# Performance work log

Hardware: AMD Instinct MI355X
Metric: run time of the kernel (lower is better)

## Reference

```python
import jax, jax.numpy as jnp
import numpy as np

B, N, D_IN, D_OUT, H = 64, 512, 256, 256, 4
HD = D_OUT // H


def setup_inputs() -> dict:
    key = jax.random.key(0)
    ks = jax.random.split(key, 10)
    x = jax.random.normal(ks[0], (B, N, D_IN), dtype=jnp.float32)
    adj = jax.random.randint(ks[1], (N, N), 0, 2, dtype=jnp.int32)
    adj = adj.at[jnp.arange(N), jnp.arange(N)].set(1)  # self-loops: no empty rows
    s_in = 1.0 / np.sqrt(D_IN)
    s_out = 1.0 / np.sqrt(D_OUT)
    wq = jax.random.uniform(ks[2], (D_OUT, D_IN), jnp.float32, -s_in, s_in)
    bq = jax.random.uniform(ks[3], (D_OUT,), jnp.float32, -s_in, s_in)
    wk = jax.random.uniform(ks[4], (D_OUT, D_IN), jnp.float32, -s_in, s_in)
    bk = jax.random.uniform(ks[5], (D_OUT,), jnp.float32, -s_in, s_in)
    wv = jax.random.uniform(ks[6], (D_OUT, D_IN), jnp.float32, -s_in, s_in)
    bv = jax.random.uniform(ks[7], (D_OUT,), jnp.float32, -s_in, s_in)
    wo = jax.random.uniform(ks[8], (D_OUT, D_OUT), jnp.float32, -s_out, s_out)
    bo = jax.random.uniform(ks[9], (D_OUT,), jnp.float32, -s_out, s_out)
    return {"x": x, "adj": adj, "wq": wq, "bq": bq, "wk": wk, "bk": bk,
            "wv": wv, "bv": bv, "wo": wo, "bo": bo}


def reference(x, adj, wq, bq, wk, bk, wv, bv, wo, bo):
    b, n, _ = x.shape
    # [B,N,D_out] -> [B,H,N,HD]
    q = (x @ wq.T + bq).reshape(b, n, H, HD).transpose(0, 2, 1, 3)
    k = (x @ wk.T + bk).reshape(b, n, H, HD).transpose(0, 2, 1, 3)
    v = (x @ wv.T + bv).reshape(b, n, H, HD).transpose(0, 2, 1, 3)
    scores = jnp.einsum('bhnd,bhmd->bhnm', q, k) / jnp.sqrt(jnp.float32(HD))
    scores = jnp.where(adj[None, None] == 0, -jnp.inf, scores)
    attn = jnp.nan_to_num(jax.nn.softmax(scores, axis=-1), nan=0.0)
    out = jnp.einsum('bhnm,bhmd->bhnd', attn, v)
    out = out.transpose(0, 2, 1, 3).reshape(b, n, D_OUT)
    return out @ wo.T + bo
```

## Files before the change

kernel.cpp:

```cpp
#include <hip/hip_runtime.h>
#include <stdint.h>

typedef float f32x4 __attribute__((ext_vector_type(4)));
typedef short s16x8 __attribute__((ext_vector_type(8)));
typedef unsigned short u16x4 __attribute__((ext_vector_type(4)));

#define BB 64
#define NN 512
#define DIN 256
#define DOUT 256
#define HH 4
#define HD 64

__device__ __forceinline__ unsigned short f2b(float f) {
  union { float f; unsigned u; } v; v.f = f;
  unsigned r = v.u + 0x7fffu + ((v.u >> 16) & 1u);
  return (unsigned short)(r >> 16);
}
__device__ __forceinline__ void mfma16(f32x4& acc, s16x8 a, s16x8 b) {
  acc = __builtin_amdgcn_mfma_f32_16x16x32_bf16(a, b, acc, 0, 0, 0);
}
__device__ __forceinline__ unsigned cvtpk(float lo, float hi) {
  unsigned r;
  asm("v_cvt_pk_bf16_f32 %0, %1, %2" : "=v"(r) : "v"(lo), "v"(hi));
  return r;
}

__global__ void k_conv(const float* __restrict__ src, unsigned short* __restrict__ dst, int n4) {
  int i = blockIdx.x * blockDim.x + threadIdx.x;
  if (i >= n4) return;
  f32x4 v = ((const f32x4*)src)[i];
  u16x4 o;
  o[0] = f2b(v[0]); o[1] = f2b(v[1]); o[2] = f2b(v[2]); o[3] = f2b(v[3]);
  ((u16x4*)dst)[i] = o;
}

__global__ void k_adjbits(const int* __restrict__ adj, unsigned long long* __restrict__ ab) {
  int row = blockIdx.x;
  int w = threadIdx.x >> 6, lane = threadIdx.x & 63;
  int v = adj[row * NN + w * 64 + lane];
  unsigned long long m = __ballot(v != 0);
  if (lane == 0) ab[row * 8 + w] = m;
}

__global__ __launch_bounds__(256) void k_qkv(
    const unsigned short* __restrict__ xh,
    const unsigned short* __restrict__ wqh,
    const unsigned short* __restrict__ wkh,
    const unsigned short* __restrict__ wvh,
    const float* __restrict__ bq, const float* __restrict__ bk, const float* __restrict__ bv,
    unsigned short* __restrict__ Qb, unsigned short* __restrict__ Kb, unsigned short* __restrict__ Vtb)
{
  __shared__ __align__(16) unsigned char xs[32768];
  __shared__ __align__(16) unsigned char wsl[32768];
  int tid = threadIdx.x, wave = tid >> 6, lane = tid & 63;
  int lr = lane & 15, lk = lane >> 4;
  int t0 = blockIdx.x * 64;
  int by = blockIdx.y, seg = by >> 2, nb0 = (by & 3) * 64;
  const unsigned short* wh = seg == 0 ? wqh : (seg == 1 ? wkh : wvh);
  const float* bias = seg == 0 ? bq : (seg == 1 ? bk : bv);
  int h = by & 3;

  const unsigned short* xsrc = xh + (size_t)t0 * DIN;
  const unsigned short* wsrc = wh + (size_t)nb0 * DIN;
#pragma unroll
  for (int i = 0; i < 8; ++i) {
    int lin = i * 256 + tid;
    int r = lin >> 5, c = lin & 31;
    int dst = r * 512 + ((c ^ (r & 7)) << 4);
    *(s16x8*)(xs + dst)  = *(const s16x8*)(xsrc + lin * 8);
    *(s16x8*)(wsl + dst) = *(const s16x8*)(wsrc + lin * 8);
  }
  __syncthreads();

  f32x4 acc[4] = {};
  if (seg < 2) {
    int chrow = wave * 16 + lr;
#pragma unroll
    for (int k0 = 0; k0 < 8; ++k0) {
      int cg = k0 * 4 + lk;
      s16x8 a = *(const s16x8*)(wsl + chrow * 512 + ((cg ^ (chrow & 7)) << 4));
#pragma unroll
      for (int ct = 0; ct < 4; ++ct) {
        int tr = ct * 16 + lr;
        s16x8 b = *(const s16x8*)(xs + tr * 512 + ((cg ^ (tr & 7)) << 4));
        mfma16(acc[ct], a, b);
      }
    }
    unsigned short* dst = (seg == 0) ? Qb : Kb;
    f32x4 bv4 = *(const f32x4*)(bias + nb0 + wave * 16 + lk * 4);
#pragma unroll
    for (int ct = 0; ct < 4; ++ct) {
      int n_ = t0 + ct * 16 + lr;
      int b_ = n_ >> 9, nn = n_ & 511;
      u16x4 pk;
#pragma unroll
      for (int j = 0; j < 4; ++j) pk[j] = f2b(acc[ct][j] + bv4[j]);
      *(u16x4*)(dst + ((size_t)(b_ * HH + h) * NN + nn) * HD + wave * 16 + lk * 4) = pk;
    }
  } else {
    int tokrow = wave * 16 + lr;
#pragma unroll
    for (int k0 = 0; k0 < 8; ++k0) {
      int cg = k0 * 4 + lk;
      s16x8 a = *(const s16x8*)(xs + tokrow * 512 + ((cg ^ (tokrow & 7)) << 4));
#pragma unroll
      for (int nt = 0; nt < 4; ++nt) {
        int cr = nt * 16 + lr;
        s16x8 b = *(const s16x8*)(wsl + cr * 512 + ((cg ^ (cr & 7)) << 4));
        mfma16(acc[nt], a, b);
      }
    }
    int m0 = t0 + wave * 16 + lk * 4;
    int b_ = m0 >> 9, n0 = m0 & 511;
#pragma unroll
    for (int nt = 0; nt < 4; ++nt) {
      int hd = nt * 16 + lr;
      float bs = bias[nb0 + hd];
      u16x4 pk;
#pragma unroll
      for (int j = 0; j < 4; ++j) pk[j] = f2b(acc[nt][j] + bs);
      *(u16x4*)(Vtb + ((size_t)(b_ * HH + h) * HD + hd) * NN + n0) = pk;
    }
  }
}

__global__ __launch_bounds__(256) void k_attn(
    const unsigned short* __restrict__ Qb, const unsigned short* __restrict__ Kb,
    const unsigned short* __restrict__ Vtb, const unsigned long long* __restrict__ ab,
    unsigned short* __restrict__ att)
{
  __shared__ __align__(16) unsigned char kl[8192];
  __shared__ __align__(16) unsigned char vtl[8192];
  __shared__ __align__(16) unsigned char plb[8192];

  int tid = threadIdx.x, wave = tid >> 6, lane = tid & 63;
  int lr = lane & 15, lk = lane >> 4;
  int qt = blockIdx.x;
  int bh = blockIdx.y;
  int h = bh & 3, b_ = bh >> 2;
  const unsigned short* Qp = Qb + (size_t)bh * NN * HD;
  const unsigned short* Kp = Kb + (size_t)bh * NN * HD;
  const unsigned short* Vp = Vtb + (size_t)bh * HD * NN;
  int q0 = qt * 64 + wave * 16;

  s16x8 qa0 = *(const s16x8*)(Qp + (q0 + lr) * HD + lk * 8);
  s16x8 qa1 = *(const s16x8*)(Qp + (q0 + lr) * HD + 32 + lk * 8);

  f32x4 oacc[4] = {};
  float rs = 0.f;
  unsigned char* plw = plb + wave * 2048;
  int sw = (lr & 7) << 4;

  for (int kt = 0; kt < 8; ++kt) {
    for (int i = tid; i < 1024; i += 256) {
      if (i < 512) {
        int r = i >> 3, c = i & 7;
        s16x8 v = *(const s16x8*)(Kp + (kt * 64 + r) * HD + c * 8);
        *(s16x8*)(kl + r * 128 + ((c * 16) ^ ((r & 7) << 4))) = v;
      } else {
        int i2 = i - 512;
        int d = i2 >> 3, c = i2 & 7;
        s16x8 v = *(const s16x8*)(Vp + d * NN + kt * 64 + c * 8);
        *(s16x8*)(vtl + d * 128 + ((c * 16) ^ ((d & 7) << 4))) = v;
      }
    }
    __syncthreads();

    unsigned long long abr = ab[(size_t)(q0 + lr) * 8 + kt];

#pragma unroll
    for (int ks = 0; ks < 4; ++ks) {
      int key = ks * 16 + lr;
      s16x8 kb0 = *(const s16x8*)(kl + key * 128 + ((lk * 16) ^ ((key & 7) << 4)));
      s16x8 kb1 = *(const s16x8*)(kl + key * 128 + ((64 + lk * 16) ^ ((key & 7) << 4)));
      f32x4 s = {};
      mfma16(s, kb0, qa0);
      mfma16(s, kb1, qa1);
      float p[4];
#pragma unroll
      for (int j = 0; j < 4; ++j)
        p[j] = ((abr >> (ks * 16 + lk * 4 + j)) & 1ULL) ? __expf(s[j] * 0.125f) : 0.0f;
      unsigned w0 = cvtpk(p[0], p[1]);
      unsigned w1 = cvtpk(p[2], p[3]);
      union { unsigned u; float f; } t0, t1, t2, t3;
      t0.u = w0 << 16; t1.u = w0 & 0xffff0000u;
      t2.u = w1 << 16; t3.u = w1 & 0xffff0000u;
      rs += (t0.f + t1.f) + (t2.f + t3.f);
      uint2 pw; pw.x = w0; pw.y = w1;
      *(uint2*)(plw + lr * 128 + ((ks * 32 + lk * 8) ^ sw)) = pw;
    }
    __syncthreads();

    s16x8 pa0 = *(const s16x8*)(plw + lr * 128 + ((lk * 16) ^ sw));
    s16x8 pa1 = *(const s16x8*)(plw + lr * 128 + ((64 + lk * 16) ^ sw));
#pragma unroll
    for (int dt = 0; dt < 4; ++dt) {
      int d = dt * 16 + lr;
      s16x8 vb0 = *(const s16x8*)(vtl + d * 128 + ((lk * 16) ^ ((d & 7) << 4)));
      s16x8 vb1 = *(const s16x8*)(vtl + d * 128 + ((64 + lk * 16) ^ ((d & 7) << 4)));
      mfma16(oacc[dt], vb0, pa0);
      mfma16(oacc[dt], vb1, pa1);
    }
    __syncthreads();
  }

  rs += __shfl_xor(rs, 16);
  rs += __shfl_xor(rs, 32);
  float rinv = 1.0f / rs;

  int n_ = q0 + lr;
#pragma unroll
  for (int dt = 0; dt < 4; ++dt) {
    uint2 ow;
    ow.x = cvtpk(oacc[dt][0] * rinv, oacc[dt][1] * rinv);
    ow.y = cvtpk(oacc[dt][2] * rinv, oacc[dt][3] * rinv);
    *(uint2*)(att + ((size_t)(b_ * NN + n_) * DOUT) + h * HD + dt * 16 + lk * 4) = ow;
  }
}

__global__ __launch_bounds__(256) void k_out(
    const unsigned short* __restrict__ att, const unsigned short* __restrict__ woh,
    const float* __restrict__ bo, float* __restrict__ out)
{
  __shared__ __align__(16) unsigned char as_[32768];
  __shared__ __align__(16) unsigned char wsl[32768];
  int tid = threadIdx.x, wave = tid >> 6, lane = tid & 63;
  int lr = lane & 15, lk = lane >> 4;
  int t0 = blockIdx.x * 64;
  int nb0 = blockIdx.y * 64;

  const unsigned short* asrc = att + (size_t)t0 * DOUT;
  const unsigned short* wsrc = woh + (size_t)nb0 * DOUT;
#pragma unroll
  for (int i = 0; i < 8; ++i) {
    int lin = i * 256 + tid;
    int r = lin >> 5, c = lin & 31;
    int dst = r * 512 + ((c ^ (r & 7)) << 4);
    *(s16x8*)(as_ + dst) = *(const s16x8*)(asrc + lin * 8);
    *(s16x8*)(wsl + dst) = *(const s16x8*)(wsrc + lin * 8);
  }
  __syncthreads();

  f32x4 acc[4] = {};
  int chrow = wave * 16 + lr;
#pragma unroll
  for (int k0 = 0; k0 < 8; ++k0) {
    int cg = k0 * 4 + lk;
    s16x8 a = *(const s16x8*)(wsl + chrow * 512 + ((cg ^ (chrow & 7)) << 4));
#pragma unroll
    for (int ct = 0; ct < 4; ++ct) {
      int tr = ct * 16 + lr;
      s16x8 b = *(const s16x8*)(as_ + tr * 512 + ((cg ^ (tr & 7)) << 4));
      mfma16(acc[ct], a, b);
    }
  }
  f32x4 bv4 = *(const f32x4*)(bo + nb0 + wave * 16 + lk * 4);
#pragma unroll
  for (int ct = 0; ct < 4; ++ct) {
    int m = t0 + ct * 16 + lr;
    f32x4 o = acc[ct] + bv4;
    *(f32x4*)(out + (size_t)m * DOUT + nb0 + wave * 16 + lk * 4) = o;
  }
}

extern "C" void kernel_launch(void* const* d_in, const int* in_sizes, int n_in,
                              void* d_out, int out_size, void* d_ws, size_t ws_size,
                              hipStream_t stream) {
  const float* x  = (const float*)d_in[0];
  const int*   adj = (const int*)d_in[1];
  const float* wq = (const float*)d_in[2];
  const float* bq = (const float*)d_in[3];
  const float* wk = (const float*)d_in[4];
  const float* bk = (const float*)d_in[5];
  const float* wv = (const float*)d_in[6];
  const float* bv = (const float*)d_in[7];
  const float* wo = (const float*)d_in[8];
  const float* bo = (const float*)d_in[9];
  float* out = (float*)d_out;

  char* ws = (char*)d_ws;
  size_t off = 0;
  auto carve = [&](size_t bytes) -> char* {
    off = (off + 255) & ~(size_t)255;
    char* p = ws + off;
    off += bytes;
    return p;
  };
  unsigned short* xh   = (unsigned short*)carve((size_t)BB * NN * DIN * 2);
  unsigned short* wqh  = (unsigned short*)carve((size_t)DOUT * DIN * 2);
  unsigned short* wkh  = (unsigned short*)carve((size_t)DOUT * DIN * 2);
  unsigned short* wvh  = (unsigned short*)carve((size_t)DOUT * DIN * 2);
  unsigned short* woh  = (unsigned short*)carve((size_t)DOUT * DOUT * 2);
  unsigned long long* abits = (unsigned long long*)carve((size_t)NN * 8 * 8);
  unsigned short* Qb   = (unsigned short*)carve((size_t)BB * HH * NN * HD * 2);
  unsigned short* Kb   = (unsigned short*)carve((size_t)BB * HH * NN * HD * 2);
  unsigned short* Vtb  = (unsigned short*)carve((size_t)BB * HH * HD * NN * 2);
  unsigned short* attb = (unsigned short*)carve((size_t)BB * NN * DOUT * 2);

  k_conv<<<dim3(8192), 256, 0, stream>>>(x, xh, (BB * NN * DIN) / 4);
  k_conv<<<dim3(64), 256, 0, stream>>>(wq, wqh, (DOUT * DIN) / 4);
  k_conv<<<dim3(64), 256, 0, stream>>>(wk, wkh, (DOUT * DIN) / 4);
  k_conv<<<dim3(64), 256, 0, stream>>>(wv, wvh, (DOUT * DIN) / 4);
  k_conv<<<dim3(64), 256, 0, stream>>>(wo, woh, (DOUT * DOUT) / 4);
  k_adjbits<<<dim3(512), 512, 0, stream>>>(adj, abits);
  k_qkv<<<dim3(512, 12), 256, 0, stream>>>(xh, wqh, wkh, wvh, bq, bk, bv, Qb, Kb, Vtb);
  k_attn<<<dim3(8, 256), 256, 0, stream>>>(Qb, Kb, Vtb, abits, attb);
  k_out<<<dim3(512, 4), 256, 0, stream>>>(attb, woh, bo, out);
}
```

Measured before the change: 214.2 us.

## Enlarge attention blocks to 512 threads with two query strips per wave

The attention kernel now runs 512-thread blocks covering 256 queries per (batch, head), with each wave holding two 16-row query strips. Each K/V tile staged in LDS is reused across four times as many queries, and a flat grid maps consecutive blocks to neighbouring heads, which changes cache locality. The staging loop becomes one load per thread for K and V, and the mid-iteration barrier is dropped because each wave reads only its own P buffer. The cost is more registers per wave, a larger P buffer in LDS, and only 512 blocks, which may leave occupancy and load balance worse on a large GPU.

```diff
diff --git a/kernel.cpp b/kernel.cpp
--- a/kernel.cpp
+++ b/kernel.cpp
@@ -125,97 +125,104 @@
   }
 }
 
-__global__ __launch_bounds__(256) void k_attn(
+__global__ __launch_bounds__(512, 4) void k_attn(
     const unsigned short* __restrict__ Qb, const unsigned short* __restrict__ Kb,
     const unsigned short* __restrict__ Vtb, const unsigned long long* __restrict__ ab,
     unsigned short* __restrict__ att)
 {
   __shared__ __align__(16) unsigned char kl[8192];
   __shared__ __align__(16) unsigned char vtl[8192];
-  __shared__ __align__(16) unsigned char plb[8192];
+  __shared__ __align__(16) unsigned char plb[32768];
 
   int tid = threadIdx.x, wave = tid >> 6, lane = tid & 63;
   int lr = lane & 15, lk = lane >> 4;
-  int qt = blockIdx.x;
-  int bh = blockIdx.y;
+  int bid = blockIdx.x;
+  int g = bid >> 4, r = bid & 15;
+  int bh = g * 8 + (r & 7);
+  int qt = r >> 3;
   int h = bh & 3, b_ = bh >> 2;
   const unsigned short* Qp = Qb + (size_t)bh * NN * HD;
   const unsigned short* Kp = Kb + (size_t)bh * NN * HD;
   const unsigned short* Vp = Vtb + (size_t)bh * HD * NN;
-  int q0 = qt * 64 + wave * 16;
-
-  s16x8 qa0 = *(const s16x8*)(Qp + (q0 + lr) * HD + lk * 8);
-  s16x8 qa1 = *(const s16x8*)(Qp + (q0 + lr) * HD + 32 + lk * 8);
-
-  f32x4 oacc[4] = {};
-  float rs = 0.f;
-  unsigned char* plw = plb + wave * 2048;
+  int q0 = qt * 256 + wave * 32;
+
+  s16x8 qa[2][2];
+#pragma unroll
+  for (int s = 0; s < 2; ++s) {
+    qa[s][0] = *(const s16x8*)(Qp + (q0 + s * 16 + lr) * HD + lk * 8);
+    qa[s][1] = *(const s16x8*)(Qp + (q0 + s * 16 + lr) * HD + 32 + lk * 8);
+  }
+
+  f32x4 oacc[2][4] = {};
+  float rs[2] = {0.f, 0.f};
+  unsigned char* plw = plb + wave * 4096;
   int sw = (lr & 7) << 4;
 
+  int srow = tid >> 3, scol = tid & 7;
+  int sdst = srow * 128 + ((scol * 16) ^ ((srow & 7) << 4));
+
   for (int kt = 0; kt < 8; ++kt) {
-    for (int i = tid; i < 1024; i += 256) {
-      if (i < 512) {
-        int r = i >> 3, c = i & 7;
-        s16x8 v = *(const s16x8*)(Kp + (kt * 64 + r) * HD + c * 8);
-        *(s16x8*)(kl + r * 128 + ((c * 16) ^ ((r & 7) << 4))) = v;
-      } else {
-        int i2 = i - 512;
-        int d = i2 >> 3, c = i2 & 7;
-        s16x8 v = *(const s16x8*)(Vp + d * NN + kt * 64 + c * 8);
-        *(s16x8*)(vtl + d * 128 + ((c * 16) ^ ((d & 7) << 4))) = v;
+    *(s16x8*)(kl + sdst)  = *(const s16x8*)(Kp + (kt * 64 + srow) * HD + scol * 8);
+    *(s16x8*)(vtl + sdst) = *(const s16x8*)(Vp + srow * NN + kt * 64 + scol * 8);
+    unsigned long long abr[2];
+#pragma unroll
+    for (int s = 0; s < 2; ++s) abr[s] = ab[(size_t)(q0 + s * 16 + lr) * 8 + kt];
+    __syncthreads();
+
+#pragma unroll
+    for (int s = 0; s < 2; ++s) {
+#pragma unroll
+      for (int ks = 0; ks < 4; ++ks) {
+        int key = ks * 16 + lr;
+        s16x8 kb0 = *(const s16x8*)(kl + key * 128 + ((lk * 16) ^ ((key & 7) << 4)));
+        s16x8 kb1 = *(const s16x8*)(kl + key * 128 + ((64 + lk * 16) ^ ((key & 7) << 4)));
+        f32x4 sx = {};
+        mfma16(sx, kb0, qa[s][0]);
+        mfma16(sx, kb1, qa[s][1]);
+        float p[4];
+#pragma unroll
+        for (int j = 0; j < 4; ++j)
+          p[j] = ((abr[s] >> (ks * 16 + lk * 4 + j)) & 1ULL) ? __expf(sx[j] * 0.125f) : 0.0f;
+        unsigned w0 = cvtpk(p[0], p[1]);
+        unsigned w1 = cvtpk(p[2], p[3]);
+        union { unsigned u; float f; } t0, t1, t2, t3;
+        t0.u = w0 << 16; t1.u = w0 & 0xffff0000u;
+        t2.u = w1 << 16; t3.u = w1 & 0xffff0000u;
+        rs[s] += (t0.f + t1.f) + (t2.f + t3.f);
+        uint2 pw; pw.x = w0; pw.y = w1;
+        *(uint2*)(plw + s * 2048 + lr * 128 + ((ks * 32 + lk * 8) ^ sw)) = pw;
       }
     }
+#pragma unroll
+    for (int s = 0; s < 2; ++s) {
+      s16x8 pa0 = *(const s16x8*)(plw + s * 2048 + lr * 128 + ((lk * 16) ^ sw));
+      s16x8 pa1 = *(const s16x8*)(plw + s * 2048 + lr * 128 + ((64 + lk * 16) ^ sw));
+#pragma unroll
+      for (int dt = 0; dt < 4; ++dt) {
+        int d = dt * 16 + lr;
+        s16x8 vb0 = *(const s16x8*)(vtl + d * 128 + ((lk * 16) ^ ((d & 7) << 4)));
+        s16x8 vb1 = *(const s16x8*)(vtl + d * 128 + ((64 + lk * 16) ^ ((d & 7) << 4)));
+        mfma16(oacc[s][dt], vb0, pa0);
+        mfma16(oacc[s][dt], vb1, pa1);
+      }
+    }
     __syncthreads();
-
-    unsigned long long abr = ab[(size_t)(q0 + lr) * 8 + kt];
-
-#pragma unroll
-    for (int ks = 0; ks < 4; ++ks) {
-      int key = ks * 16 + lr;
-      s16x8 kb0 = *(const s16x8*)(kl + key * 128 + ((lk * 16) ^ ((key & 7) << 4)));
-      s16x8 kb1 = *(const s16x8*)(kl + key * 128 + ((64 + lk * 16) ^ ((key & 7) << 4)));
-      f32x4 s = {};
-      mfma16(s, kb0, qa0);
-      mfma16(s, kb1, qa1);
-      float p[4];
-#pragma unroll
-      for (int j = 0; j < 4; ++j)
-        p[j] = ((abr >> (ks * 16 + lk * 4 + j)) & 1ULL) ? __expf(s[j] * 0.125f) : 0.0f;
-      unsigned w0 = cvtpk(p[0], p[1]);
-      unsigned w1 = cvtpk(p[2], p[3]);
-      union { unsigned u; float f; } t0, t1, t2, t3;
-      t0.u = w0 << 16; t1.u = w0 & 0xffff0000u;
-      t2.u = w1 << 16; t3.u = w1 & 0xffff0000u;
-      rs += (t0.f + t1.f) + (t2.f + t3.f);
-      uint2 pw; pw.x = w0; pw.y = w1;
-      *(uint2*)(plw + lr * 128 + ((ks * 32 + lk * 8) ^ sw)) = pw;
-    }
-    __syncthreads();
-
-    s16x8 pa0 = *(const s16x8*)(plw + lr * 128 + ((lk * 16) ^ sw));
-    s16x8 pa1 = *(const s16x8*)(plw + lr * 128 + ((64 + lk * 16) ^ sw));
+  }
+
+#pragma unroll
+  for (int s = 0; s < 2; ++s) {
+    float v = rs[s];
+    v += __shfl_xor(v, 16);
+    v += __shfl_xor(v, 32);
+    float rinv = 1.0f / v;
+    int n_ = q0 + s * 16 + lr;
 #pragma unroll
     for (int dt = 0; dt < 4; ++dt) {
-      int d = dt * 16 + lr;
-      s16x8 vb0 = *(const s16x8*)(vtl + d * 128 + ((lk * 16) ^ ((d & 7) << 4)));
-      s16x8 vb1 = *(const s16x8*)(vtl + d * 128 + ((64 + lk * 16) ^ ((d & 7) << 4)));
-      mfma16(oacc[dt], vb0, pa0);
-      mfma16(oacc[dt], vb1, pa1);
-    }
-    __syncthreads();
-  }
-
-  rs += __shfl_xor(rs, 16);
-  rs += __shfl_xor(rs, 32);
-  float rinv = 1.0f / rs;
-
-  int n_ = q0 + lr;
-#pragma unroll
-  for (int dt = 0; dt < 4; ++dt) {
-    uint2 ow;
-    ow.x = cvtpk(oacc[dt][0] * rinv, oacc[dt][1] * rinv);
-    ow.y = cvtpk(oacc[dt][2] * rinv, oacc[dt][3] * rinv);
-    *(uint2*)(att + ((size_t)(b_ * NN + n_) * DOUT) + h * HD + dt * 16 + lk * 4) = ow;
+      uint2 ow;
+      ow.x = cvtpk(oacc[s][dt][0] * rinv, oacc[s][dt][1] * rinv);
+      ow.y = cvtpk(oacc[s][dt][2] * rinv, oacc[s][dt][3] * rinv);
+      *(uint2*)(att + ((size_t)(b_ * NN + n_) * DOUT) + h * HD + dt * 16 + lk * 4) = ow;
+    }
   }
 }
 
@@ -305,6 +312,6 @@
   k_conv<<<dim3(64), 256, 0, stream>>>(wo, woh, (DOUT * DOUT) / 4);
   k_adjbits<<<dim3(512), 512, 0, stream>>>(adj, abits);
   k_qkv<<<dim3(512, 12), 256, 0, stream>>>(xh, wqh, wkh, wvh, bq, bk, bv, Qb, Kb, Vtb);
-  k_attn<<<dim3(8, 256), 256, 0, stream>>>(Qb, Kb, Vtb, abits, attb);
+  k_attn<<<dim3(512), 512, 0, stream>>>(Qb, Kb, Vtb, abits, attb);
   k_out<<<dim3(512, 4), 256, 0, stream>>>(attb, woh, bo, out);
 }
```

New measurement: 210.7 us. Within noise of the previous version (-1.6%).
